# Optimization experiments

Hardware: AMD Instinct MI355X
Metric: run time of the kernel (lower is better)

The kernel has to match this reference:

```python
import jax, jax.numpy as jnp
import numpy as np

C = 512        # concept_num
D = 256        # input_dim / embedding_dim
H = 512        # msg_hidden_dim
M = 256        # msg_output_dim
OH = 512       # hidden_dim
T = 2          # edge_type_num
E = C * (C - 1)  # fully-connected graph without self-loops = 261632


def _glorot(key, shape, fan_in):
    return jax.random.normal(key, shape, jnp.float32) / np.sqrt(fan_in).astype(np.float32)


def setup_inputs() -> dict:
    key = jax.random.key(0)
    ks = jax.random.split(key, 12)
    inputs = jax.random.normal(ks[0], (C, D), jnp.float32)
    rel_type = jax.random.uniform(ks[1], (E, T), jnp.float32)
    send_idx = jax.random.randint(ks[2], (E,), 0, C, jnp.int32)
    rec_idx = jax.random.randint(ks[3], (E,), 0, C, jnp.int32)
    # per-edge-type message MLP params, stacked over type dim
    W1 = _glorot(ks[4], (T, 2 * D, H), 2 * D)
    b1 = jnp.zeros((T, H), jnp.float32)
    W2 = _glorot(ks[5], (T, H, M), H)
    b2 = jnp.zeros((T, M), jnp.float32)
    # output MLP params
    Wo1 = _glorot(ks[6], (M, OH), M)
    bo1 = jnp.zeros((OH,), jnp.float32)
    Wo2 = _glorot(ks[7], (OH, OH), OH)
    bo2 = jnp.zeros((OH,), jnp.float32)
    Wo3 = _glorot(ks[8], (OH, D), OH)
    bo3 = jnp.zeros((D,), jnp.float32)
    return {"inputs": inputs, "rel_type": rel_type, "W1": W1, "b1": b1,
            "W2": W2, "b2": b2, "Wo1": Wo1, "bo1": bo1, "Wo2": Wo2,
            "bo2": bo2, "Wo3": Wo3, "bo3": bo3,
            "send_idx": send_idx, "rec_idx": rec_idx}


def reference(inputs, rel_type, W1, b1, W2, b2, Wo1, bo1, Wo2, bo2, Wo3, bo3,
              send_idx, rec_idx):
    # node2edge: one-hot sparse matmul == index gather
    senders = jnp.take(inputs, send_idx, axis=0)      # [E, D]
    receivers = jnp.take(inputs, rec_idx, axis=0)     # [E, D]
    pre_msg = jnp.concatenate([senders, receivers], axis=-1)  # [E, 2D]
    # per-edge-type MLPs, weighted-summed by rel_type (dropout=0 / eval mode)
    all_msgs = jnp.zeros((pre_msg.shape[0], M), jnp.float32)
    for i in range(T):
        msg = jax.nn.relu(pre_msg @ W1[i] + b1[i])    # [E, H]
        msg = jax.nn.relu(msg @ W2[i] + b2[i])        # [E, M]
        all_msgs = all_msgs + msg * rel_type[:, i:i + 1]
    # edge2node: transposed one-hot sparse matmul == scatter-add over receivers
    agg_msgs = jax.ops.segment_sum(all_msgs, rec_idx, num_segments=inputs.shape[0])  # [C, M]
    pred = jax.nn.relu(agg_msgs @ Wo1 + bo1)
    pred = jax.nn.relu(pred @ Wo2 + bo2)
    return pred @ Wo3 + bo3                           # [C, D]
```

## Files before the change

### kernel.cpp

```cpp
#include <hip/hip_runtime.h>

#define C_N   512
#define E_N   261632
#define CAP   768

typedef _Float16 f16;
typedef _Float16 f16x8_t __attribute__((ext_vector_type(8)));
typedef float    f32x16_t __attribute__((ext_vector_type(16)));

__global__ __launch_bounds__(256) void k_prep_all(
    const float* __restrict__ inputs, const float* __restrict__ W1,
    const float* __restrict__ b1, const float* __restrict__ W2,
    const float* __restrict__ Wo1, const float* __restrict__ Wo2, const float* __restrict__ Wo3,
    f16* __restrict__ SA, f16* __restrict__ RB, f16* __restrict__ W2p,
    f16* __restrict__ Wo1p, f16* __restrict__ Wo2p, f16* __restrict__ Wo3p,
    int* __restrict__ cnt, float* __restrict__ agg)
{
  __shared__ f16 wt[2][256][18];
  int bid = blockIdx.x;
  int tid = threadIdx.x;
  if (bid < 64) {
    int lane = tid & 63, w = tid >> 6;
    int hlf = lane >> 5, l31 = lane & 31;
    int br = bid & 7, bc = (bid >> 3) & 1, mi = bid >> 4;
    int t = mi >> 1, half = mi & 1;
    const float* Wsrc = W1 + (size_t)t * 512 * 512 + (size_t)half * 256 * 512;

    f32x16_t acc[2][2];
    #pragma unroll
    for (int rt = 0; rt < 2; rt++)
      #pragma unroll
      for (int ctl = 0; ctl < 2; ctl++)
        #pragma unroll
        for (int r = 0; r < 16; r++) acc[rt][ctl][r] = 0.f;

    #pragma unroll
    for (int i = 0; i < 4; i++) {
      int idx = tid + i * 256;
      int k = idx >> 6, n4 = idx & 63;
      float4 v = *(const float4*)&Wsrc[(size_t)k * 512 + bc * 256 + n4 * 4];
      wt[0][n4 * 4 + 0][k] = (f16)v.x;
      wt[0][n4 * 4 + 1][k] = (f16)v.y;
      wt[0][n4 * 4 + 2][k] = (f16)v.z;
      wt[0][n4 * 4 + 3][k] = (f16)v.w;
    }

    for (int kc = 0; kc < 16; kc++) {
      __syncthreads();
      if (kc + 1 < 16) {
        int b = (kc + 1) & 1;
        #pragma unroll
        for (int i = 0; i < 4; i++) {
          int idx = tid + i * 256;
          int k = idx >> 6, n4 = idx & 63;
          float4 v = *(const float4*)&Wsrc[(size_t)((kc + 1) * 16 + k) * 512 + bc * 256 + n4 * 4];
          wt[b][n4 * 4 + 0][k] = (f16)v.x;
          wt[b][n4 * 4 + 1][k] = (f16)v.y;
          wt[b][n4 * 4 + 2][k] = (f16)v.z;
          wt[b][n4 * 4 + 3][k] = (f16)v.w;
        }
      }
      f16x8_t af[2];
      #pragma unroll
      for (int rt = 0; rt < 2; rt++) {
        const float4* p = (const float4*)&inputs[(size_t)(br * 64 + rt * 32 + l31) * 256 + kc * 16 + hlf * 8];
        float4 u0 = p[0], u1 = p[1];
        af[rt] = (f16x8_t){(f16)u0.x, (f16)u0.y, (f16)u0.z, (f16)u0.w,
                           (f16)u1.x, (f16)u1.y, (f16)u1.z, (f16)u1.w};
      }
      int b = kc & 1;
      #pragma unroll
      for (int ctl = 0; ctl < 2; ctl++) {
        int n = (2 * w + ctl) * 32 + l31;
        f16x8_t bfr = *(const f16x8_t*)&wt[b][n][hlf * 8];
        #pragma unroll
        for (int rt = 0; rt < 2; rt++)
          acc[rt][ctl] = __builtin_amdgcn_mfma_f32_32x32x16_f16(af[rt], bfr, acc[rt][ctl], 0, 0, 0);
      }
    }
    f16* dst = (half == 0) ? SA : RB;
    #pragma unroll
    for (int ctl = 0; ctl < 2; ctl++) {
      int col = bc * 256 + (2 * w + ctl) * 32 + l31;
      float bias = (half == 1) ? b1[t * 512 + col] : 0.f;
      #pragma unroll
      for (int rt = 0; rt < 2; rt++)
        #pragma unroll
        for (int r = 0; r < 16; r++) {
          int row = br * 64 + rt * 32 + (r & 3) + 8 * (r >> 2) + 4 * hlf;
          dst[((size_t)(t * 512 + row)) * 512 + col] = (f16)(acc[rt][ctl][r] + bias);
        }
    }
  } else if (bid < 192) {
    int gid  = (bid - 64) * 256 + tid;
    int lane = gid & 63;
    int ct   = (gid >> 6) & 7;
    int kc   = (gid >> 9) & 31;
    int t    = gid >> 14;
    int n    = ct * 32 + (lane & 31);
    int k0   = kc * 16 + (lane >> 5) * 8;
    const float* src = W2 + (size_t)t * 512 * 256;
    f16x8_t v;
    #pragma unroll
    for (int j = 0; j < 8; j++) v[j] = (f16)src[(size_t)(k0 + j) * 256 + n];
    *(f16x8_t*)(W2p + (size_t)gid * 8) = v;
  } else if (bid < 256) {
    int gid  = (bid - 192) * 256 + tid;
    int lane = gid & 63;
    int ct   = (gid >> 6) & 15;
    int kc   = gid >> 10;
    int n    = ct * 32 + (lane & 31);
    int k0   = kc * 16 + (lane >> 5) * 8;
    f16x8_t v;
    #pragma unroll
    for (int j = 0; j < 8; j++) v[j] = (f16)Wo1[(size_t)(k0 + j) * 512 + n];
    *(f16x8_t*)(Wo1p + (size_t)gid * 8) = v;
  } else if (bid < 384) {
    int gid  = (bid - 256) * 256 + tid;
    int lane = gid & 63;
    int ct   = (gid >> 6) & 15;
    int kc   = gid >> 10;
    int n    = ct * 32 + (lane & 31);
    int k0   = kc * 16 + (lane >> 5) * 8;
    f16x8_t v;
    #pragma unroll
    for (int j = 0; j < 8; j++) v[j] = (f16)Wo2[(size_t)(k0 + j) * 512 + n];
    *(f16x8_t*)(Wo2p + (size_t)gid * 8) = v;
  } else if (bid < 448) {
    int gid  = (bid - 384) * 256 + tid;
    int lane = gid & 63;
    int ct   = (gid >> 6) & 7;
    int kc   = gid >> 9;
    int n    = ct * 32 + (lane & 31);
    int k0   = kc * 16 + (lane >> 5) * 8;
    f16x8_t v;
    #pragma unroll
    for (int j = 0; j < 8; j++) v[j] = (f16)Wo3[(size_t)(k0 + j) * 256 + n];
    *(f16x8_t*)(Wo3p + (size_t)gid * 8) = v;
  } else if (bid == 448) {
    for (int i = tid; i < 512 * 16; i += 256) cnt[i] = 0;
  } else {
    float4* a4 = (float4*)agg;
    for (int i = tid; i < 512 * 64; i += 256) a4[i] = make_float4(0.f, 0.f, 0.f, 0.f);
  }
}

__global__ __launch_bounds__(512) void k_scatter_d(const int* __restrict__ rec,
    const int* __restrict__ send, const float* __restrict__ rel,
    int* __restrict__ cnt, uint2* __restrict__ smeta)
{
  __shared__ int lh[512];
  __shared__ int lb[512];
  int b = blockIdx.x;
  int e0 = b * (E_N / 128);
  lh[threadIdx.x] = 0;
  __syncthreads();
  for (int i = threadIdx.x; i < E_N / 128; i += 512)
    atomicAdd(&lh[rec[e0 + i]], 1);
  __syncthreads();
  {
    int c = lh[threadIdx.x];
    lb[threadIdx.x] = c ? atomicAdd(&cnt[threadIdx.x * 16], c) : 0;
    lh[threadIdx.x] = 0;
  }
  __syncthreads();
  for (int i = threadIdx.x; i < E_N / 128; i += 512) {
    int e = e0 + i;
    int r = rec[e];
    int p = r * CAP + lb[r] + atomicAdd(&lh[r], 1);
    f16 r0 = (f16)rel[2 * (size_t)e];
    f16 r1 = (f16)rel[2 * (size_t)e + 1];
    unsigned pk = ((unsigned)__builtin_bit_cast(unsigned short, r1) << 16)
                |  (unsigned)__builtin_bit_cast(unsigned short, r0);
    smeta[p] = make_uint2((unsigned)send[e], pk);
  }
}

#define H1S 136

__global__ __launch_bounds__(512, 4) void k_edges(
    const f16* __restrict__ SA, const f16* __restrict__ RB,
    const f16* __restrict__ W2p, const float* __restrict__ b2,
    const uint2* __restrict__ smeta, const int* __restrict__ cnt,
    float* __restrict__ agg)
{
  __shared__ f16   h1[2][128][H1S];
  __shared__ f16   rbs[2][512];
  __shared__ float b2s[2][256];
  __shared__ float aggL[2][256];
  __shared__ __align__(16) float relv[2][128];
  __shared__ int   sends[128];

  int c   = blockIdx.x;
  int ti  = blockIdx.y;
  int n_c = cnt[c * 16];
  if (ti * 128 >= n_c) return;

  int tid  = threadIdx.x;
  int lane = tid & 63;
  int w    = tid >> 6;
  int hlf  = lane >> 5;
  int l31  = lane & 31;
  int q4   = tid & 15;
  int rb0  = tid >> 4;
  int rg   = w >> 2;
  int cg   = w & 3;

  if (tid < 128) {
    int t = tid >> 6, qq = tid & 63;
    *(f16x8_t*)&rbs[t][qq * 8] = *(const f16x8_t*)&RB[((size_t)(t * 512 + c)) * 512 + qq * 8];
  }
  ((float*)aggL)[tid] = 0.f;
  { int t = (tid >> 8) & 1, col = tid & 255; b2s[t][col] = b2[t * 256 + col]; }

  int s0 = c * CAP + ti * 128;
  int nv = n_c - ti * 128; if (nv > 128) nv = 128;

  if (tid < 128) {
    if (tid < nv) {
      uint2 m = smeta[s0 + tid];
      sends[tid] = (int)m.x;
      relv[0][tid] = (float)__builtin_bit_cast(f16, (unsigned short)(m.y & 0xffffu));
      relv[1][tid] = (float)__builtin_bit_cast(f16, (unsigned short)(m.y >> 16));
    } else {
      sends[tid] = 0; relv[0][tid] = 0.f; relv[1][tid] = 0.f;
    }
  }
  __syncthreads();

  const f16x8_t* SAc = (const f16x8_t*)SA;
  const f16x8_t* Bp  = (const f16x8_t*)W2p;

  const f16 fz = (f16)0.f;
  const f16x8_t z8 = {fz, fz, fz, fz, fz, fz, fz, fz};

  int voff[4];
  #pragma unroll
  for (int j = 0; j < 4; j++)
    voff[j] = sends[rb0 + 32 * j] * 64 + q4;

  f16x8_t g[4];

  #pragma unroll
  for (int j = 0; j < 4; j++) g[j] = SAc[voff[j]];
  {
    f16x8_t rbq = *(const f16x8_t*)&rbs[0][q4 * 8];
    #pragma unroll
    for (int j = 0; j < 4; j++) {
      f16x8_t sv = g[j] + rbq;
      sv = __builtin_elementwise_max(sv, z8);
      *(f16x8_t*)&h1[0][rb0 + 32 * j][q4 * 8] = sv;
    }
  }

  f32x16_t acc[2][2];

  for (int p = 0; p < 8; p++) {
    int t  = p >> 2;
    int ks = p & 3;
    int pb = p & 1;
    __syncthreads();

    if (p < 7) {
      int off = ((p + 1) >> 2) * 32768 + ((p + 1) & 3) * 16;
      #pragma unroll
      for (int j = 0; j < 4; j++) g[j] = SAc[voff[j] + off];
    }

    if (ks == 0) {
      #pragma unroll
      for (int a = 0; a < 2; a++)
        #pragma unroll
        for (int b_ = 0; b_ < 2; b_++)
          #pragma unroll
          for (int r = 0; r < 16; r++) acc[a][b_][r] = 0.f;
    }

    const f16x8_t* Bw = Bp + ((size_t)((t * 32 + ks * 8) * 8 + cg * 2) * 64 + lane);

    f16x8_t bb[2][2];
    bb[0][0] = Bw[0];    bb[0][1] = Bw[64];
    bb[1][0] = Bw[512];  bb[1][1] = Bw[512 + 64];

    const f16* h1b = &h1[pb][0][0];
    int a0 = (rg * 64 + l31) * H1S + hlf * 8;
    #pragma unroll
    for (int kc = 0; kc < 8; kc++) {
      int qb = kc & 1;
      f16x8_t af0 = *(const f16x8_t*)&h1b[a0 + kc * 16];
      f16x8_t af1 = *(const f16x8_t*)&h1b[a0 + 32 * H1S + kc * 16];
      acc[0][0] = __builtin_amdgcn_mfma_f32_32x32x16_f16(af0, bb[qb][0], acc[0][0], 0, 0, 0);
      acc[0][1] = __builtin_amdgcn_mfma_f32_32x32x16_f16(af0, bb[qb][1], acc[0][1], 0, 0, 0);
      acc[1][0] = __builtin_amdgcn_mfma_f32_32x32x16_f16(af1, bb[qb][0], acc[1][0], 0, 0, 0);
      acc[1][1] = __builtin_amdgcn_mfma_f32_32x32x16_f16(af1, bb[qb][1], acc[1][1], 0, 0, 0);
      if (kc + 2 < 8) {
        bb[qb][0] = Bw[(kc + 2) * 512];
        bb[qb][1] = Bw[(kc + 2) * 512 + 64];
      }
    }

    if (ks == 3) {
      #pragma unroll
      for (int ctl = 0; ctl < 2; ctl++) {
        int col = (cg * 2 + ctl) * 32 + l31;
        float b2c = b2s[t][col];
        float csum = 0.f;
        #pragma unroll
        for (int rt = 0; rt < 2; rt++) {
          int rbase = rg * 64 + rt * 32 + 4 * hlf;
          #pragma unroll
          for (int grp = 0; grp < 4; grp++) {
            float4 rv = *(const float4*)&relv[t][rbase + 8 * grp];
            float v0 = fmaxf(acc[rt][ctl][grp * 4 + 0] + b2c, 0.f);
            float v1 = fmaxf(acc[rt][ctl][grp * 4 + 1] + b2c, 0.f);
            float v2 = fmaxf(acc[rt][ctl][grp * 4 + 2] + b2c, 0.f);
            float v3 = fmaxf(acc[rt][ctl][grp * 4 + 3] + b2c, 0.f);
            csum += v0 * rv.x + v1 * rv.y + v2 * rv.z + v3 * rv.w;
          }
        }
        csum += __shfl_xor(csum, 32, 64);
        if (hlf == 0) aggL[rg][col] += csum;
      }
    }

    if (p < 7) {
      int tn = (p + 1) >> 2, ksn = (p + 1) & 3;
      f16x8_t rbq = *(const f16x8_t*)&rbs[tn][ksn * 128 + q4 * 8];
      #pragma unroll
      for (int j = 0; j < 4; j++) {
        f16x8_t sv = g[j] + rbq;
        sv = __builtin_elementwise_max(sv, z8);
        *(f16x8_t*)&h1[pb ^ 1][rb0 + 32 * j][q4 * 8] = sv;
      }
    }
  }

  __syncthreads();

  if (tid < 256) atomicAdd(&agg[(size_t)c * 256 + tid], aggL[0][tid] + aggL[1][tid]);
}

#define HOS 520

__global__ __launch_bounds__(1024, 4) void k_omlp(const float* __restrict__ agg,
    const f16* __restrict__ Wo1p, const float* __restrict__ bo1,
    const f16* __restrict__ Wo2p, const float* __restrict__ bo2,
    const f16* __restrict__ Wo3p, const float* __restrict__ bo3,
    float* __restrict__ out)
{
  __shared__ f16 hL1[32 * HOS];
  __shared__ f16 hL2[32 * HOS];
  int tid = threadIdx.x, lane = tid & 63, w = tid >> 6;
  int hlf = lane >> 5, l31 = lane & 31;
  int br = blockIdx.x;

  {
    f32x16_t acc;
    #pragma unroll
    for (int r = 0; r < 16; r++) acc[r] = 0.f;
    for (int kc = 0; kc < 16; kc++) {
      const float4* p = (const float4*)&agg[(size_t)(br * 32 + l31) * 256 + kc * 16 + hlf * 8];
      float4 u0 = p[0], u1 = p[1];
      f16x8_t af = (f16x8_t){(f16)u0.x, (f16)u0.y, (f16)u0.z, (f16)u0.w,
                             (f16)u1.x, (f16)u1.y, (f16)u1.z, (f16)u1.w};
      f16x8_t bfr = *(const f16x8_t*)&Wo1p[((size_t)(kc * 16 + w) * 64 + lane) * 8];
      acc = __builtin_amdgcn_mfma_f32_32x32x16_f16(af, bfr, acc, 0, 0, 0);
    }
    int col = w * 32 + l31;
    float bias = bo1[col];
    #pragma unroll
    for (int r = 0; r < 16; r++) {
      int row = (r & 3) + 8 * (r >> 2) + 4 * hlf;
      hL1[row * HOS + col] = (f16)fmaxf(acc[r] + bias, 0.f);
    }
  }
  __syncthreads();

  {
    f32x16_t acc;
    #pragma unroll
    for (int r = 0; r < 16; r++) acc[r] = 0.f;
    for (int kc = 0; kc < 32; kc++) {
      f16x8_t af  = *(const f16x8_t*)&hL1[l31 * HOS + kc * 16 + hlf * 8];
      f16x8_t bfr = *(const f16x8_t*)&Wo2p[((size_t)(kc * 16 + w) * 64 + lane) * 8];
      acc = __builtin_amdgcn_mfma_f32_32x32x16_f16(af, bfr, acc, 0, 0, 0);
    }
    int col = w * 32 + l31;
    float bias = bo2[col];
    #pragma unroll
    for (int r = 0; r < 16; r++) {
      int row = (r & 3) + 8 * (r >> 2) + 4 * hlf;
      hL2[row * HOS + col] = (f16)fmaxf(acc[r] + bias, 0.f);
    }
  }
  __syncthreads();

  if (w < 8) {
    f32x16_t acc;
    #pragma unroll
    for (int r = 0; r < 16; r++) acc[r] = 0.f;
    for (int kc = 0; kc < 32; kc++) {
      f16x8_t af  = *(const f16x8_t*)&hL2[l31 * HOS + kc * 16 + hlf * 8];
      f16x8_t bfr = *(const f16x8_t*)&Wo3p[((size_t)(kc * 8 + w) * 64 + lane) * 8];
      acc = __builtin_amdgcn_mfma_f32_32x32x16_f16(af, bfr, acc, 0, 0, 0);
    }
    int col = w * 32 + l31;
    float bias = bo3[col];
    #pragma unroll
    for (int r = 0; r < 16; r++) {
      int row = br * 32 + (r & 3) + 8 * (r >> 2) + 4 * hlf;
      out[(size_t)row * 256 + col] = acc[r] + bias;
    }
  }
}

extern "C" void kernel_launch(void* const* d_in, const int* in_sizes, int n_in,
                              void* d_out, int out_size, void* d_ws, size_t ws_size,
                              hipStream_t stream)
{
  (void)in_sizes; (void)n_in; (void)out_size; (void)ws_size;
  const float* inputs = (const float*)d_in[0];
  const float* rel    = (const float*)d_in[1];
  const float* W1     = (const float*)d_in[2];
  const float* b1     = (const float*)d_in[3];
  const float* W2     = (const float*)d_in[4];
  const float* b2     = (const float*)d_in[5];
  const float* Wo1    = (const float*)d_in[6];
  const float* bo1    = (const float*)d_in[7];
  const float* Wo2    = (const float*)d_in[8];
  const float* bo2    = (const float*)d_in[9];
  const float* Wo3    = (const float*)d_in[10];
  const float* bo3    = (const float*)d_in[11];
  const int* send_idx = (const int*)d_in[12];
  const int* rec_idx  = (const int*)d_in[13];
  float* out = (float*)d_out;

  char* ws = (char*)d_ws;
  f16*    SA    = (f16*)   (ws);
  f16*    RB    = (f16*)   (ws + (1024u << 10));
  f16*    W2p   = (f16*)   (ws + (2048u << 10));
  float*  agg   = (float*) (ws + (2560u << 10));
  int*    cnt   = (int*)   (ws + (3072u << 10));
  f16*    Wo1p  = (f16*)   (ws + (3136u << 10));
  f16*    Wo2p  = (f16*)   (ws + (3392u << 10));
  f16*    Wo3p  = (f16*)   (ws + (3904u << 10));
  uint2*  smeta = (uint2*) (ws + (4160u << 10));

  k_prep_all <<<dim3(450),    dim3(256),  0, stream>>>(inputs, W1, b1, W2, Wo1, Wo2, Wo3,
                                                       SA, RB, W2p, Wo1p, Wo2p, Wo3p, cnt, agg);
  k_scatter_d<<<dim3(128),    dim3(512),  0, stream>>>(rec_idx, send_idx, rel, cnt, smeta);
  k_edges    <<<dim3(512, 5), dim3(512),  0, stream>>>(SA, RB, W2p, b2, smeta, cnt, agg);
  k_omlp     <<<dim3(16),     dim3(1024), 0, stream>>>(agg, Wo1p, bo1, Wo2p, bo2, Wo3p, bo3, out);
}
```

Before: 298.2 us.

## Load edge-MLP A fragments directly from global, dropping LDS h1 staging

Removes the shared-memory h1 double buffer and per-stage barriers in the edge kernel. Each wave gathers its sender rows of the first-layer table straight from global memory, adds the receiver bias and applies ReLU in registers right before the MFMAs. This cuts LDS usage and synchronisation, which may raise occupancy, at the cost of duplicated global gathers across the column-group waves and more exposed load latency inside the MFMA loop.

```diff
diff --git a/kernel.cpp b/kernel.cpp
--- a/kernel.cpp
+++ b/kernel.cpp
@@ -176,15 +176,12 @@
   }
 }
 
-#define H1S 136
-
 __global__ __launch_bounds__(512, 4) void k_edges(
     const f16* __restrict__ SA, const f16* __restrict__ RB,
     const f16* __restrict__ W2p, const float* __restrict__ b2,
     const uint2* __restrict__ smeta, const int* __restrict__ cnt,
     float* __restrict__ agg)
 {
-  __shared__ f16   h1[2][128][H1S];
   __shared__ f16   rbs[2][512];
   __shared__ float b2s[2][256];
   __shared__ float aggL[2][256];
@@ -201,8 +198,6 @@
   int w    = tid >> 6;
   int hlf  = lane >> 5;
   int l31  = lane & 31;
-  int q4   = tid & 15;
-  int rb0  = tid >> 4;
   int rg   = w >> 2;
   int cg   = w & 3;
 
@@ -228,44 +223,20 @@
   }
   __syncthreads();
 
+  int srow0 = sends[rg * 64 + l31];
+  int srow1 = sends[rg * 64 + 32 + l31];
+
   const f16x8_t* SAc = (const f16x8_t*)SA;
   const f16x8_t* Bp  = (const f16x8_t*)W2p;
 
   const f16 fz = (f16)0.f;
   const f16x8_t z8 = {fz, fz, fz, fz, fz, fz, fz, fz};
-
-  int voff[4];
-  #pragma unroll
-  for (int j = 0; j < 4; j++)
-    voff[j] = sends[rb0 + 32 * j] * 64 + q4;
-
-  f16x8_t g[4];
-
-  #pragma unroll
-  for (int j = 0; j < 4; j++) g[j] = SAc[voff[j]];
-  {
-    f16x8_t rbq = *(const f16x8_t*)&rbs[0][q4 * 8];
-    #pragma unroll
-    for (int j = 0; j < 4; j++) {
-      f16x8_t sv = g[j] + rbq;
-      sv = __builtin_elementwise_max(sv, z8);
-      *(f16x8_t*)&h1[0][rb0 + 32 * j][q4 * 8] = sv;
-    }
-  }
 
   f32x16_t acc[2][2];
 
   for (int p = 0; p < 8; p++) {
     int t  = p >> 2;
     int ks = p & 3;
-    int pb = p & 1;
-    __syncthreads();
-
-    if (p < 7) {
-      int off = ((p + 1) >> 2) * 32768 + ((p + 1) & 3) * 16;
-      #pragma unroll
-      for (int j = 0; j < 4; j++) g[j] = SAc[voff[j] + off];
-    }
 
     if (ks == 0) {
       #pragma unroll
@@ -276,19 +247,28 @@
           for (int r = 0; r < 16; r++) acc[a][b_][r] = 0.f;
     }
 
+    int abase0 = (t * 512 + srow0) * 64 + ks * 16 + hlf;
+    int abase1 = (t * 512 + srow1) * 64 + ks * 16 + hlf;
+
     const f16x8_t* Bw = Bp + ((size_t)((t * 32 + ks * 8) * 8 + cg * 2) * 64 + lane);
 
     f16x8_t bb[2][2];
     bb[0][0] = Bw[0];    bb[0][1] = Bw[64];
     bb[1][0] = Bw[512];  bb[1][1] = Bw[512 + 64];
 
-    const f16* h1b = &h1[pb][0][0];
-    int a0 = (rg * 64 + l31) * H1S + hlf * 8;
+    f16x8_t ga0 = SAc[abase0];
+    f16x8_t ga1 = SAc[abase1];
+
     #pragma unroll
     for (int kc = 0; kc < 8; kc++) {
       int qb = kc & 1;
-      f16x8_t af0 = *(const f16x8_t*)&h1b[a0 + kc * 16];
-      f16x8_t af1 = *(const f16x8_t*)&h1b[a0 + 32 * H1S + kc * 16];
+      f16x8_t rbq = *(const f16x8_t*)&rbs[t][ks * 128 + kc * 16 + hlf * 8];
+      f16x8_t af0 = __builtin_elementwise_max(ga0 + rbq, z8);
+      f16x8_t af1 = __builtin_elementwise_max(ga1 + rbq, z8);
+      if (kc < 7) {
+        ga0 = SAc[abase0 + (kc + 1) * 2];
+        ga1 = SAc[abase1 + (kc + 1) * 2];
+      }
       acc[0][0] = __builtin_amdgcn_mfma_f32_32x32x16_f16(af0, bb[qb][0], acc[0][0], 0, 0, 0);
       acc[0][1] = __builtin_amdgcn_mfma_f32_32x32x16_f16(af0, bb[qb][1], acc[0][1], 0, 0, 0);
       acc[1][0] = __builtin_amdgcn_mfma_f32_32x32x16_f16(af1, bb[qb][0], acc[1][0], 0, 0, 0);
@@ -320,17 +300,6 @@
         }
         csum += __shfl_xor(csum, 32, 64);
         if (hlf == 0) aggL[rg][col] += csum;
-      }
-    }
-
-    if (p < 7) {
-      int tn = (p + 1) >> 2, ksn = (p + 1) & 3;
-      f16x8_t rbq = *(const f16x8_t*)&rbs[tn][ksn * 128 + q4 * 8];
-      #pragma unroll
-      for (int j = 0; j < 4; j++) {
-        f16x8_t sv = g[j] + rbq;
-        sv = __builtin_elementwise_max(sv, z8);
-        *(f16x8_t*)&h1[pb ^ 1][rb0 + 32 * j][q4 * 8] = sv;
       }
     }
   }
```

Measured after the change: 459.4 us. 1.54x slower.
